# Kernel optimization log

Measured on AMD Instinct MI355X. Metric: run time of the kernel, lower is better.

The kernel has to match this reference:

```python
import jax, jax.numpy as jnp
import numpy as np
import math

H = 8
D_MODEL = 32
D_HEAD = 4
FACTOR = 5
EPS = 1e-5

DATANUM = 1024
B = 512            # outer batch; becomes attention sequence length
C = 32
L = DATANUM // 8   # 128; becomes attention batch
U = min(FACTOR * int(math.ceil(math.log(B))), B)  # 35 (U_part == u since L_Q == L_K == B)


def setup_inputs() -> dict:
    key = jax.random.key(0)
    ks = jax.random.split(key, 16)
    s = 0.05
    return {
        'x': jax.random.normal(ks[0], (B, C, L), jnp.float32),
        'Wq': jax.random.normal(ks[1], (D_MODEL, D_MODEL), jnp.float32) * s,
        'bq': jnp.zeros((D_MODEL,), jnp.float32),
        'Wk': jax.random.normal(ks[2], (D_MODEL, D_MODEL), jnp.float32) * s,
        'bk': jnp.zeros((D_MODEL,), jnp.float32),
        'Wv': jax.random.normal(ks[3], (D_MODEL, D_MODEL), jnp.float32) * s,
        'bv': jnp.zeros((D_MODEL,), jnp.float32),
        'Wo': jax.random.normal(ks[4], (D_MODEL, D_MODEL), jnp.float32) * s,
        'bo': jnp.zeros((D_MODEL,), jnp.float32),
        'bn1_gamma': jnp.ones((C,), jnp.float32),
        'bn1_beta': jnp.zeros((C,), jnp.float32),
        'bn1_mean': jnp.zeros((C,), jnp.float32),
        'bn1_var': jnp.ones((C,), jnp.float32),
        'W1': jax.random.normal(ks[5], (DATANUM * 8, DATANUM * 4), jnp.float32) * 0.01,
        'b1': jnp.zeros((DATANUM * 8,), jnp.float32),
        'W2': jax.random.normal(ks[6], (DATANUM * 4, DATANUM * 8), jnp.float32) * 0.01,
        'b2': jnp.zeros((DATANUM * 4,), jnp.float32),
        'bn2_gamma': jnp.ones((C,), jnp.float32),
        'bn2_beta': jnp.zeros((C,), jnp.float32),
        'bn2_mean': jnp.zeros((C,), jnp.float32),
        'bn2_var': jnp.ones((C,), jnp.float32),
        'index_sample': jax.random.randint(ks[7], (B, U), 0, B, jnp.int64),
    }


def _bn(x, gamma, beta, mean, var):
    # eval-mode BatchNorm1d over channel dim of (batch, C, length)
    inv = jax.lax.rsqrt(var + EPS)
    return (x - mean[None, :, None]) * (inv * gamma)[None, :, None] + beta[None, :, None]


def _prob_attention(Q, K, V, index_sample):
    # Q,K,V: (Ba, H, Lq, D) self-attention, Lq == Lk. Informer ProbAttention, mask_flag=True.
    Ba, Hh, Lq, D = Q.shape
    u = index_sample.shape[1]
    # sparsity measurement on sampled keys
    K_sample = K[:, :, index_sample, :]                       # (Ba,H,Lq,U,D)
    QK_sample = jnp.einsum('bhld,bhlud->bhlu', Q, K_sample)
    M = QK_sample.max(axis=-1) - QK_sample.sum(axis=-1) / Lq  # (Ba,H,Lq)
    _, M_top = jax.lax.top_k(M, u)                            # (Ba,H,u) selected queries
    Q_reduce = jnp.take_along_axis(Q, M_top[..., None], axis=2)  # (Ba,H,u,D)
    scores = jnp.einsum('bhud,bhkd->bhuk', Q_reduce, K) / jnp.sqrt(jnp.float32(D))
    # ProbMask: causal w.r.t. the selected query's original position
    causal = jnp.arange(Lq)[None, None, None, :] > M_top[..., None]
    scores = jnp.where(causal, -jnp.inf, scores)
    attn = jax.nn.softmax(scores, axis=-1)
    upd = jnp.einsum('bhuk,bhkd->bhud', attn, V)              # (Ba,H,u,D)
    context = jnp.cumsum(V, axis=2)                           # initial context (mask_flag=True)
    b_idx = jnp.arange(Ba)[:, None, None]
    h_idx = jnp.arange(Hh)[None, :, None]
    context = context.at[b_idx, h_idx, M_top].set(upd)
    return context


def reference(x, Wq, bq, Wk, bk, Wv, bv, Wo, bo,
              bn1_gamma, bn1_beta, bn1_mean, bn1_var,
              W1, b1, W2, b2,
              bn2_gamma, bn2_beta, bn2_mean, bn2_var,
              index_sample):
    Bsz, Cc, Ll = x.shape
    res1 = x
    xa = jnp.transpose(x, (2, 0, 1))                          # (L, B, 32): attn batch=L, seq=B

    def heads(t):
        return jnp.transpose(t.reshape(Ll, Bsz, H, D_HEAD), (0, 2, 1, 3))

    Q = heads(xa @ Wq.T + bq)
    K = heads(xa @ Wk.T + bk)
    V = heads(xa @ Wv.T + bv)
    ctx = _prob_attention(Q, K, V, index_sample)              # (L,H,B,D)
    out = jnp.transpose(ctx, (0, 2, 1, 3)).reshape(Ll, Bsz, D_MODEL)
    out = out @ Wo.T + bo
    xh = jax.nn.relu(out)                                     # dropout = identity (eval)
    xh = jnp.transpose(xh, (1, 2, 0))                         # (B,32,L)
    xh = _bn(xh + res1, bn1_gamma, bn1_beta, bn1_mean, bn1_var)
    res2 = xh
    f = xh.reshape(Bsz, Cc * Ll)
    f = jax.nn.relu(f @ W1.T + b1)
    f = jax.nn.relu(f @ W2.T + b2)
    f = f.reshape(Bsz, Cc, Ll)
    return _bn(f + res2, bn2_gamma, bn2_beta, bn2_mean, bn2_var)
```

## Files before the change

kernel.cpp:

```cpp
#include <hip/hip_runtime.h>
#include <stdint.h>

#define EPSF 1e-5f
#define NEG_INF (-1e30f)

typedef float f32x4 __attribute__((ext_vector_type(4)));
typedef __bf16 bf16x8 __attribute__((ext_vector_type(8)));
typedef unsigned short u16x8 __attribute__((ext_vector_type(8)));

typedef __attribute__((address_space(3))) unsigned char* as3_ptr;
typedef const __attribute__((address_space(1))) unsigned char* as1_ptr;

__device__ __forceinline__ void async16(const void* g, void* l) {
  __builtin_amdgcn_global_load_lds((as1_ptr)g, (as3_ptr)l, 16, 0, 0);
}

__device__ __forceinline__ unsigned short f2bf(float f) {
  union { float f; unsigned int u; } v; v.f = f;
  unsigned int r = v.u + 0x7FFFu + ((v.u >> 16) & 1u);
  return (unsigned short)(r >> 16);
}
__device__ __forceinline__ unsigned short f2bf_fast(float f) {
  union { float f; unsigned int u; } v; v.f = f;
  return (unsigned short)((v.u + 0x8000u) >> 16);
}

__global__ __launch_bounds__(256) void transpose_k(const float* __restrict__ src,
                                                   float* __restrict__ dst, int R, int C) {
  __shared__ float tl[32][33];
  int tx = threadIdx.x & 31, ty = threadIdx.x >> 5;
  int c0 = blockIdx.x * 32, r0 = blockIdx.y * 32;
#pragma unroll
  for (int i = 0; i < 4; i++)
    tl[ty + i * 8][tx] = src[(size_t)(r0 + ty + i * 8) * C + c0 + tx];
  __syncthreads();
#pragma unroll
  for (int i = 0; i < 4; i++)
    dst[(size_t)(c0 + ty + i * 8) * R + r0 + tx] = tl[tx][ty + i * 8];
}

__global__ __launch_bounds__(256) void qkv_k(const float* __restrict__ xT,
    const float* __restrict__ Wq, const float* __restrict__ bq,
    const float* __restrict__ Wk, const float* __restrict__ bk,
    const float* __restrict__ Wv, const float* __restrict__ bv,
    float* __restrict__ Q, float* __restrict__ Kq, float* __restrict__ Vq) {
  __shared__ float xs[64 * 33];
  __shared__ float wq[32 * 33], wk[32 * 33], wvs[32 * 33];
  __shared__ float bqs[32], bks[32], bvs[32];
  int tid = threadIdx.x;
  int a = blockIdx.x;
  int tbase = blockIdx.y * 256;
#pragma unroll
  for (int i = 0; i < 4; i++) {
    int e = i * 256 + tid; int r = e >> 5, c = e & 31;
    wq[r * 33 + c] = Wq[e]; wk[r * 33 + c] = Wk[e]; wvs[r * 33 + c] = Wv[e];
  }
  if (tid < 32) { bqs[tid] = bq[tid]; bks[tid] = bk[tid]; bvs[tid] = bv[tid]; }
  int tl = tid & 63, rg = tid >> 6;
  for (int ch = 0; ch < 4; ch++) {
    __syncthreads();
#pragma unroll
    for (int i = 0; i < 8; i++) {
      int e = i * 256 + tid; int r = e >> 5, c = e & 31;
      xs[r * 33 + c] = xT[(size_t)a * 16384 + (size_t)(tbase + ch * 64) * 32 + e];
    }
    __syncthreads();
    float qa[8], ka[8], va[8];
#pragma unroll
    for (int r8 = 0; r8 < 8; r8++) {
      int r = rg * 8 + r8; qa[r8] = bqs[r]; ka[r8] = bks[r]; va[r8] = bvs[r];
    }
    for (int c = 0; c < 32; c++) {
      float xv = xs[tl * 33 + c];
#pragma unroll
      for (int r8 = 0; r8 < 8; r8++) {
        int r = rg * 8 + r8;
        qa[r8] += xv * wq[r * 33 + c];
        ka[r8] += xv * wk[r * 33 + c];
        va[r8] += xv * wvs[r * 33 + c];
      }
    }
    int t = tbase + ch * 64 + tl;
#pragma unroll
    for (int r8 = 0; r8 < 8; r8++) {
      int r = rg * 8 + r8;
      size_t o = (size_t)a * 16384 + (size_t)r * 512 + t;
      Q[o] = qa[r8]; Kq[o] = ka[r8]; Vq[o] = va[r8];
    }
  }
}

__global__ __launch_bounds__(512) void topk_k(const float* __restrict__ Q,
    const float* __restrict__ Kq, const int* __restrict__ idxs,
    int* __restrict__ Mtop, int U) {
  __shared__ float Ks[2048];
  __shared__ float Ml[512];
  __shared__ float rv[8];
  __shared__ int ri[8];
  int bh = blockIdx.x;
  int tid = threadIdx.x, lane = tid & 63, wv = tid >> 6;
  size_t base = (size_t)bh * 2048;
#pragma unroll
  for (int i = 0; i < 4; i++) Ks[i * 512 + tid] = Kq[base + i * 512 + tid];
  float q0 = Q[base + tid], q1 = Q[base + 512 + tid];
  float q2 = Q[base + 1024 + tid], q3 = Q[base + 1536 + tid];
  __syncthreads();
  float mx = NEG_INF, sm = 0.f;
  for (int u = 0; u < U; u++) {
    int it = idxs[tid * U + u];
    it = min(max(it, 0), 511);
    float s = q0 * Ks[it] + q1 * Ks[512 + it] + q2 * Ks[1024 + it] + q3 * Ks[1536 + it];
    mx = fmaxf(mx, s); sm += s;
  }
  Ml[tid] = mx - sm * (1.f / 512.f);
  __syncthreads();
  for (int s_i = 0; s_i < U; s_i++) {
    float v = Ml[tid]; int ii = tid;
#pragma unroll
    for (int off = 32; off; off >>= 1) {
      float ov = __shfl_xor(v, off); int oi = __shfl_xor(ii, off);
      if (ov > v || (ov == v && oi < ii)) { v = ov; ii = oi; }
    }
    if (lane == 0) { rv[wv] = v; ri[wv] = ii; }
    __syncthreads();
    if (tid == 0) {
      float bv = rv[0]; int bi = ri[0];
      for (int w = 1; w < 8; w++)
        if (rv[w] > bv || (rv[w] == bv && ri[w] < bi)) { bv = rv[w]; bi = ri[w]; }
      Mtop[bh * U + s_i] = bi;
      Ml[bi] = NEG_INF;
    }
    __syncthreads();
  }
}

__global__ __launch_bounds__(256) void attn_k(const float* __restrict__ Q,
    const float* __restrict__ Kq, const float* __restrict__ Vq,
    const int* __restrict__ Mtop, float* __restrict__ Ctx, int U) {
  __shared__ float Ks[2048];
  __shared__ float Vs[2048];
  __shared__ int mt[64];
  __shared__ float Qr[64][4];
  __shared__ float upd[64][4];
  int bh = blockIdx.x;
  int tid = threadIdx.x, lane = tid & 63, wv = tid >> 6;
  size_t base = (size_t)bh * 2048;
#pragma unroll
  for (int i = 0; i < 8; i++) {
    Ks[i * 256 + tid] = Kq[base + i * 256 + tid];
    Vs[i * 256 + tid] = Vq[base + i * 256 + tid];
  }
  if (tid < U) mt[tid] = Mtop[bh * U + tid];
  __syncthreads();
  if (tid < 4 * U) { int u = tid >> 2, d = tid & 3; Qr[u][d] = Q[base + d * 512 + mt[u]]; }
  __syncthreads();
  for (int u = wv; u < U; u += 4) {
    int mrow = mt[u];
    float q0 = Qr[u][0], q1 = Qr[u][1], q2 = Qr[u][2], q3 = Qr[u][3];
    float sv[8]; float lmax = NEG_INF;
#pragma unroll
    for (int jj = 0; jj < 8; jj++) {
      int k = jj * 64 + lane;
      float s = NEG_INF;
      if (k <= mrow)
        s = 0.5f * (q0 * Ks[k] + q1 * Ks[512 + k] + q2 * Ks[1024 + k] + q3 * Ks[1536 + k]);
      sv[jj] = s; lmax = fmaxf(lmax, s);
    }
#pragma unroll
    for (int off = 32; off; off >>= 1) lmax = fmaxf(lmax, __shfl_xor(lmax, off));
    float ls = 0.f, p0 = 0.f, p1 = 0.f, p2 = 0.f, p3 = 0.f;
#pragma unroll
    for (int jj = 0; jj < 8; jj++) {
      int k = jj * 64 + lane;
      if (k <= mrow) {
        float p = __expf(sv[jj] - lmax);
        ls += p; p0 += p * Vs[k]; p1 += p * Vs[512 + k];
        p2 += p * Vs[1024 + k]; p3 += p * Vs[1536 + k];
      }
    }
#pragma unroll
    for (int off = 32; off; off >>= 1) {
      ls += __shfl_xor(ls, off); p0 += __shfl_xor(p0, off); p1 += __shfl_xor(p1, off);
      p2 += __shfl_xor(p2, off); p3 += __shfl_xor(p3, off);
    }
    if (lane == 0) {
      float inv = 1.f / ls;
      upd[u][0] = p0 * inv; upd[u][1] = p1 * inv; upd[u][2] = p2 * inv; upd[u][3] = p3 * inv;
    }
  }
  __syncthreads();
  {
    float v[8];
    int b0 = wv * 512 + lane * 8;
#pragma unroll
    for (int q = 0; q < 8; q++) v[q] = Vs[b0 + q];
#pragma unroll
    for (int q = 1; q < 8; q++) v[q] += v[q - 1];
    float x = v[7];
    for (int off = 1; off < 64; off <<= 1) {
      float y = __shfl_up(x, off);
      if (lane >= off) x += y;
    }
    float excl = x - v[7];
#pragma unroll
    for (int q = 0; q < 8; q++) Vs[b0 + q] = v[q] + excl;
  }
  __syncthreads();
  if (tid < 4 * U) { int u = tid >> 2, d = tid & 3; Vs[d * 512 + mt[u]] = upd[u][d]; }
  __syncthreads();
#pragma unroll
  for (int i = 0; i < 8; i++) Ctx[base + i * 256 + tid] = Vs[i * 256 + tid];
}

__global__ __launch_bounds__(256) void oproj_k(const float* __restrict__ Ctx,
    const float* __restrict__ Wo, const float* __restrict__ bo, float* __restrict__ Y) {
  __shared__ float cs[32 * 256];
  __shared__ float wo[32 * 33];
  __shared__ float bos[32];
  int tid = threadIdx.x;
  int a = blockIdx.x, t0 = blockIdx.y * 256;
#pragma unroll
  for (int i = 0; i < 4; i++) {
    int e = i * 256 + tid; int r = e >> 5, c = e & 31;
    wo[r * 33 + c] = Wo[e];
  }
  if (tid < 32) bos[tid] = bo[tid];
#pragma unroll
  for (int i = 0; i < 32; i++) {
    int e = i * 256 + tid; int row = e >> 8, col = e & 255;
    cs[e] = Ctx[(size_t)a * 16384 + (size_t)row * 512 + t0 + col];
  }
  __syncthreads();
  int rl = tid & 31, tw = tid >> 5;
  for (int ti = 0; ti < 32; ti++) {
    int t = ti * 8 + tw;
    float acc = bos[rl];
#pragma unroll
    for (int rp = 0; rp < 32; rp++) acc += cs[rp * 256 + t] * wo[rl * 33 + rp];
    Y[(size_t)a * 16384 + (size_t)(t0 + t) * 32 + rl] = acc;
  }
}

__global__ __launch_bounds__(256) void bn1t_k(const float* __restrict__ Y,
    const float* __restrict__ x, const float* __restrict__ g1, const float* __restrict__ be1,
    const float* __restrict__ me1, const float* __restrict__ va1,
    float* __restrict__ Xh, unsigned short* __restrict__ Fb) {
  __shared__ float tl[32][33];
  int tx = threadIdx.x & 31, ty = threadIdx.x >> 5;
  int c0 = blockIdx.x * 32;
  int r0 = blockIdx.y * 32;
#pragma unroll
  for (int i = 0; i < 4; i++)
    tl[ty + i * 8][tx] = Y[(size_t)(r0 + ty + i * 8) * 16384 + c0 + tx];
  __syncthreads();
#pragma unroll
  for (int i = 0; i < 4; i++) {
    int m = c0 + ty + i * 8;
    int a = r0 + tx;
    float v = tl[tx][ty + i * 8];
    int ch = m & 31;
    size_t oi = (size_t)m * 128 + a;
    float val = fmaxf(v, 0.f) + x[oi];
    float s = g1[ch] * rsqrtf(va1[ch] + EPSF);
    float res = (val - me1[ch]) * s + be1[ch];
    Xh[oi] = res;
    Fb[oi] = f2bf(res);
  }
}

__global__ __launch_bounds__(256) void wcvt_k(const float* __restrict__ W,
    unsigned short* __restrict__ Wb, int n4) {
  int stride = gridDim.x * 256;
  for (int idx = blockIdx.x * 256 + threadIdx.x; idx < n4; idx += stride) {
    float4 w = ((const float4*)W)[idx];
    ushort4 o;
    o.x = f2bf(w.x); o.y = f2bf(w.y); o.z = f2bf(w.z); o.w = f2bf(w.w);
    ((ushort4*)Wb)[idx] = o;
  }
}

__global__ __launch_bounds__(256, 3) void gemm_bf(
    const unsigned short* __restrict__ A, const unsigned short* __restrict__ B,
    int K, int N, int MT, int NPX, int SPLITK, float* __restrict__ P, int M) {
  __shared__ unsigned char lds[16384];
  int tid = threadIdx.x;
  int lane = tid & 63, wv = tid >> 6;
  int wm = wv >> 1, wn = wv & 1;
  int lin = blockIdx.x;
  int xcd = lin & 7, slot = lin >> 3;
  int tilesPerSp = MT * NPX;
  int sp = slot / tilesPerSp;
  int rem = slot % tilesPerSp;
  int mt = rem % MT;
  int nt = xcd * NPX + rem / MT;
  int mtile0 = mt * 128, ntile0 = nt * 128;
  int m0 = mtile0 + wm * 64, n0 = ntile0 + wn * 64;
  int frow = lane & 15, q = lane >> 4;

  int nk = K / (32 * SPLITK);
  int kbase = sp * (K / SPLITK);

  f32x4 acc[4][4];
#pragma unroll
  for (int i = 0; i < 4; i++)
#pragma unroll
    for (int j = 0; j < 4; j++) { f32x4 z = {0.f, 0.f, 0.f, 0.f}; acc[i][j] = z; }

  for (int k = 0; k < nk; k++) {
    int ks = kbase + k * 32;
#pragma unroll
    for (int i = 0; i < 2; i++) {
      int e = i * 256 + tid;
      int row = e >> 2;
      int g = (e & 3) ^ ((row >> 1) & 3);
      async16(A + (size_t)(mtile0 + row) * K + ks + g * 8, lds + i * 4096 + wv * 1024);
    }
#pragma unroll
    for (int i = 0; i < 2; i++) {
      int e = i * 256 + tid;
      int row = e >> 2;
      int g = (e & 3) ^ ((row >> 1) & 3);
      async16(B + (size_t)(ntile0 + row) * K + ks + g * 8,
              lds + 8192 + i * 4096 + wv * 1024);
    }
    __syncthreads();
    bf16x8 af[4], bfr[4];
#pragma unroll
    for (int i = 0; i < 4; i++) {
      int row = wm * 64 + i * 16 + frow;
      af[i] = *(const bf16x8*)(lds + row * 64 + ((q ^ ((row >> 1) & 3)) << 4));
    }
#pragma unroll
    for (int j = 0; j < 4; j++) {
      int row = wn * 64 + j * 16 + frow;
      bfr[j] = *(const bf16x8*)(lds + 8192 + row * 64 + ((q ^ ((row >> 1) & 3)) << 4));
    }
#pragma unroll
    for (int i = 0; i < 4; i++)
#pragma unroll
      for (int j = 0; j < 4; j++)
        acc[i][j] = __builtin_amdgcn_mfma_f32_16x16x32_bf16(af[i], bfr[j], acc[i][j], 0, 0, 0);
    __syncthreads();
  }

  float* pb = P + (size_t)sp * M * N;
#pragma unroll
  for (int i = 0; i < 4; i++)
#pragma unroll
    for (int j = 0; j < 4; j++) {
      int n = n0 + j * 16 + frow;
      int mb = m0 + i * 16 + (q << 2);
#pragma unroll
      for (int r = 0; r < 4; r++)
        pb[(size_t)(mb + r) * N + n] = acc[i][j][r];
    }
}

template <int MI, int NJ, int EPI>
__global__ __launch_bounds__(256) void gemm_ps(
    const unsigned short* __restrict__ A, const float* __restrict__ Bw,
    const float* __restrict__ bias, int K, int N, int MT, int NPX, int SPLITK,
    float* __restrict__ Pout, int M,
    unsigned short* __restrict__ Hout, const float* __restrict__ res2,
    const float* __restrict__ g2, const float* __restrict__ be2,
    const float* __restrict__ me2, const float* __restrict__ va2,
    float* __restrict__ Out) {
  constexpr int BM = MI * 32;
  constexpr int BN = NJ * 32;
  constexpr int ABYTES = BM * 32 * 2;
  constexpr int BBYTES = BN * 32 * 4;
  constexpr int SA = ABYTES / 4096;
  constexpr int SB = BBYTES / 4096;
  __shared__ unsigned char lds[ABYTES + BBYTES];
  int tid = threadIdx.x;
  int lane = tid & 63, wv = tid >> 6;
  int wm = wv >> 1, wn = wv & 1;
  int lin = blockIdx.x;
  int xcd = lin & 7, slot = lin >> 3;
  int tilesPerSp = MT * NPX;
  int sp = slot / tilesPerSp;
  int rem = slot % tilesPerSp;
  int mt = rem % MT;
  int nt = xcd * NPX + rem / MT;
  int m0 = mt * BM + wm * (BM / 2);
  int n0 = nt * BN + wn * (BN / 2);
  int frow = lane & 15, q = lane >> 4;
  int nk = K / (32 * SPLITK);
  int kbase = sp * (K / SPLITK);
  f32x4 acc[MI][NJ];
#pragma unroll
  for (int i = 0; i < MI; i++)
#pragma unroll
    for (int j = 0; j < NJ; j++) { f32x4 z = {0.f, 0.f, 0.f, 0.f}; acc[i][j] = z; }
  int mtile0 = mt * BM, ntile0 = nt * BN;
  for (int k = 0; k < nk; k++) {
    int ks = kbase + k * 32;
#pragma unroll
    for (int i = 0; i < SA; i++) {
      int e = i * 256 + tid;
      int row = e >> 2;
      int g = (e & 3) ^ ((row >> 1) & 3);
      async16(A + (size_t)(mtile0 + row) * K + ks + g * 8, lds + i * 4096 + wv * 1024);
    }
#pragma unroll
    for (int i = 0; i < SB; i++) {
      int e = i * 256 + tid;
      int row = e >> 3;
      int g = (e & 7) ^ (row & 7);
      async16(Bw + (size_t)(ntile0 + row) * K + ks + g * 4,
              lds + ABYTES + i * 4096 + wv * 1024);
    }
    __syncthreads();
    bf16x8 af[MI];
    bf16x8 bfr[NJ];
#pragma unroll
    for (int i = 0; i < MI; i++) {
      int row = wm * (BM / 2) + i * 16 + frow;
      af[i] = *(const bf16x8*)(lds + row * 64 + ((q ^ ((row >> 1) & 3)) << 4));
    }
#pragma unroll
    for (int j = 0; j < NJ; j++) {
      int row = wn * (BN / 2) + j * 16 + frow;
      const unsigned char* rb = lds + ABYTES + row * 128;
      int sw = row & 7;
      float4 w0 = *(const float4*)(rb + (((2 * q + 0) ^ sw) << 4));
      float4 w1 = *(const float4*)(rb + (((2 * q + 1) ^ sw) << 4));
      union { u16x8 u; bf16x8 b; } cv;
      cv.u[0] = f2bf_fast(w0.x); cv.u[1] = f2bf_fast(w0.y);
      cv.u[2] = f2bf_fast(w0.z); cv.u[3] = f2bf_fast(w0.w);
      cv.u[4] = f2bf_fast(w1.x); cv.u[5] = f2bf_fast(w1.y);
      cv.u[6] = f2bf_fast(w1.z); cv.u[7] = f2bf_fast(w1.w);
      bfr[j] = cv.b;
    }
#pragma unroll
    for (int i = 0; i < MI; i++)
#pragma unroll
      for (int j = 0; j < NJ; j++)
        acc[i][j] = __builtin_amdgcn_mfma_f32_16x16x32_bf16(af[i], bfr[j], acc[i][j], 0, 0, 0);
    __syncthreads();
  }
#pragma unroll
  for (int i = 0; i < MI; i++)
#pragma unroll
    for (int j = 0; j < NJ; j++) {
      int n = n0 + j * 16 + frow;
      int mb = m0 + i * 16 + (q << 2);
      if constexpr (EPI == 2) {
        float* pb = Pout + (size_t)sp * M * N;
#pragma unroll
        for (int r = 0; r < 4; r++)
          pb[(size_t)(mb + r) * N + n] = acc[i][j][r];
      } else if constexpr (EPI == 0) {
        float bb = bias[n];
#pragma unroll
        for (int r = 0; r < 4; r++) {
          float v = fmaxf(acc[i][j][r] + bb, 0.f);
          Hout[(size_t)(mb + r) * N + n] = f2bf(v);
        }
      } else {
        float bb = bias[n];
        int ch = n >> 7;
        float s = g2[ch] * rsqrtf(va2[ch] + EPSF);
        float mu = me2[ch], bt = be2[ch];
#pragma unroll
        for (int r = 0; r < 4; r++) {
          float v = fmaxf(acc[i][j][r] + bb, 0.f);
          size_t oi = (size_t)(mb + r) * N + n;
          v += res2[oi];
          Out[oi] = (v - mu) * s + bt;
        }
      }
    }
}

template <int EPI>
__global__ __launch_bounds__(256) void red_k(const float* __restrict__ P, int SP,
    const float* __restrict__ bias, const float* __restrict__ Xh,
    const float* __restrict__ g2, const float* __restrict__ be2,
    const float* __restrict__ me2, const float* __restrict__ va2,
    unsigned short* __restrict__ H, float* __restrict__ Out, int N, int MN) {
  int idx = blockIdx.x * 256 + threadIdx.x;
  const float4* p = (const float4*)P;
  int mn4 = MN >> 2;
  float4 s = p[idx];
  for (int sp = 1; sp < SP; sp++) {
    float4 t = p[idx + (size_t)sp * mn4];
    s.x += t.x; s.y += t.y; s.z += t.z; s.w += t.w;
  }
  int n = (idx << 2) & (N - 1);
  float4 bb = *(const float4*)(bias + n);
  if constexpr (EPI == 0) {
    ushort4 o;
    o.x = f2bf(fmaxf(s.x + bb.x, 0.f));
    o.y = f2bf(fmaxf(s.y + bb.y, 0.f));
    o.z = f2bf(fmaxf(s.z + bb.z, 0.f));
    o.w = f2bf(fmaxf(s.w + bb.w, 0.f));
    ((ushort4*)H)[idx] = o;
  } else {
    int ch = n >> 7;
    float sc = g2[ch] * rsqrtf(va2[ch] + EPSF);
    float mu = me2[ch], bt = be2[ch];
    float4 xh = ((const float4*)Xh)[idx];
    float4 o;
    o.x = (fmaxf(s.x + bb.x, 0.f) + xh.x - mu) * sc + bt;
    o.y = (fmaxf(s.y + bb.y, 0.f) + xh.y - mu) * sc + bt;
    o.z = (fmaxf(s.z + bb.z, 0.f) + xh.z - mu) * sc + bt;
    o.w = (fmaxf(s.w + bb.w, 0.f) + xh.w - mu) * sc + bt;
    ((float4*)Out)[idx] = o;
  }
}

extern "C" void kernel_launch(void* const* d_in, const int* in_sizes, int n_in,
                              void* d_out, int out_size, void* d_ws, size_t ws_size,
                              hipStream_t stream) {
  const float* x  = (const float*)d_in[0];
  const float* Wq = (const float*)d_in[1];  const float* bq = (const float*)d_in[2];
  const float* Wk = (const float*)d_in[3];  const float* bk = (const float*)d_in[4];
  const float* Wv = (const float*)d_in[5];  const float* bv = (const float*)d_in[6];
  const float* Wo = (const float*)d_in[7];  const float* bo = (const float*)d_in[8];
  const float* g1 = (const float*)d_in[9];  const float* be1 = (const float*)d_in[10];
  const float* me1 = (const float*)d_in[11]; const float* va1 = (const float*)d_in[12];
  const float* W1 = (const float*)d_in[13]; const float* b1 = (const float*)d_in[14];
  const float* W2 = (const float*)d_in[15]; const float* b2 = (const float*)d_in[16];
  const float* g2 = (const float*)d_in[17]; const float* be2 = (const float*)d_in[18];
  const float* me2 = (const float*)d_in[19]; const float* va2 = (const float*)d_in[20];
  const int* idxs = (const int*)d_in[21];
  int U = in_sizes[21] / 512;
  float* out = (float*)d_out;

  char* ws = (char*)d_ws;
  float* QC = (float*)(ws);
  float* Kb = (float*)(ws + (8u << 20));
  float* Vb = (float*)(ws + (16u << 20));
  float* YT = (float*)(ws + (24u << 20));
  float* Xh = (float*)(ws + (32u << 20));
  int* Mtop = (int*)(ws + (40u << 20));
  unsigned short* Fb = (unsigned short*)Vb;
  unsigned short* Hb = (unsigned short*)Kb;
  unsigned short* Wb = (unsigned short*)(ws + (48u << 20));
  float* PA = (float*)(ws + (112u << 20));
  float* P1 = (float*)(ws + (48u << 20));
  float* P2 = (float*)(ws + (80u << 20));
  bool tierA = ws_size >= (size_t)176 * (1u << 20);
  bool tierB = !tierA && ws_size >= (size_t)112 * (1u << 20);

  dim3 b256(256);
  transpose_k<<<dim3(4, 512), b256, 0, stream>>>(x, YT, 16384, 128);
  qkv_k<<<dim3(128, 2), b256, 0, stream>>>(YT, Wq, bq, Wk, bk, Wv, bv, QC, Kb, Vb);
  topk_k<<<dim3(1024), dim3(512), 0, stream>>>(QC, Kb, idxs, Mtop, U);
  attn_k<<<dim3(1024), b256, 0, stream>>>(QC, Kb, Vb, Mtop, QC, U);
  oproj_k<<<dim3(128, 2), b256, 0, stream>>>(QC, Wo, bo, YT);
  bn1t_k<<<dim3(512, 4), b256, 0, stream>>>(YT, x, g1, be1, me1, va1, Xh, Fb);

  if (tierA) {
    wcvt_k<<<dim3(2048), b256, 0, stream>>>(W1, Wb, (8192 * 4096) / 4);
    gemm_bf<<<dim3(1024), b256, 0, stream>>>(Fb, Wb, 4096, 8192, 4, 8, 4, PA, 512);
    red_k<0><<<dim3(4096), b256, 0, stream>>>(PA, 4, b1, nullptr, nullptr, nullptr,
                                              nullptr, nullptr, Hb, nullptr, 8192,
                                              512 * 8192);
    wcvt_k<<<dim3(2048), b256, 0, stream>>>(W2, Wb, (4096 * 8192) / 4);
    gemm_bf<<<dim3(1024), b256, 0, stream>>>(Hb, Wb, 8192, 4096, 4, 4, 8, PA, 512);
    red_k<1><<<dim3(2048), b256, 0, stream>>>(PA, 8, b2, Xh, g2, be2, me2, va2,
                                              nullptr, out, 4096, 512 * 4096);
  } else if (tierB) {
    gemm_ps<4, 2, 2><<<dim3(1024), b256, 0, stream>>>(
        Fb, W1, nullptr, 4096, 8192, 4, 16, 2, P1, 512,
        nullptr, nullptr, nullptr, nullptr, nullptr, nullptr, nullptr);
    red_k<0><<<dim3(4096), b256, 0, stream>>>(P1, 2, b1, nullptr, nullptr, nullptr,
                                              nullptr, nullptr, Hb, nullptr, 8192,
                                              512 * 8192);
    gemm_ps<4, 2, 2><<<dim3(1024), b256, 0, stream>>>(
        Hb, W2, nullptr, 8192, 4096, 4, 8, 4, P2, 512,
        nullptr, nullptr, nullptr, nullptr, nullptr, nullptr, nullptr);
    red_k<1><<<dim3(2048), b256, 0, stream>>>(P2, 4, b2, Xh, g2, be2, me2, va2,
                                              nullptr, out, 4096, 512 * 4096);
  } else {
    gemm_ps<4, 2, 0><<<dim3(512), b256, 0, stream>>>(
        Fb, W1, b1, 4096, 8192, 4, 16, 1, nullptr, 512,
        Hb, nullptr, nullptr, nullptr, nullptr, nullptr, nullptr);
    gemm_ps<4, 2, 1><<<dim3(256), b256, 0, stream>>>(
        Hb, W2, b2, 8192, 4096, 4, 8, 1, nullptr, 512,
        nullptr, Xh, g2, be2, me2, va2, out);
  }
}
```

Before: 590.0 us.

## Fuse top-k selection into attention kernel using rank-count selection

```diff
diff --git a/kernel.cpp b/kernel.cpp
--- a/kernel.cpp
+++ b/kernel.cpp
@@ -90,18 +90,23 @@
   }
 }
 
-__global__ __launch_bounds__(512) void topk_k(const float* __restrict__ Q,
-    const float* __restrict__ Kq, const int* __restrict__ idxs,
-    int* __restrict__ Mtop, int U) {
+__global__ __launch_bounds__(512) void topattn_k(const float* __restrict__ Q,
+    const float* __restrict__ Kq, const float* __restrict__ Vq,
+    const int* __restrict__ idxs, float* __restrict__ Ctx, int U) {
   __shared__ float Ks[2048];
+  __shared__ float Vs[2048];
   __shared__ float Ml[512];
-  __shared__ float rv[8];
-  __shared__ int ri[8];
+  __shared__ int mt[64];
+  __shared__ float Qr[64][4];
+  __shared__ float upd[64][4];
   int bh = blockIdx.x;
   int tid = threadIdx.x, lane = tid & 63, wv = tid >> 6;
   size_t base = (size_t)bh * 2048;
 #pragma unroll
-  for (int i = 0; i < 4; i++) Ks[i * 512 + tid] = Kq[base + i * 512 + tid];
+  for (int i = 0; i < 4; i++) {
+    Ks[i * 512 + tid] = Kq[base + i * 512 + tid];
+    Vs[i * 512 + tid] = Vq[base + i * 512 + tid];
+  }
   float q0 = Q[base + tid], q1 = Q[base + 512 + tid];
   float q2 = Q[base + 1024 + tid], q3 = Q[base + 1536 + tid];
   __syncthreads();
@@ -114,56 +119,29 @@
   }
   Ml[tid] = mx - sm * (1.f / 512.f);
   __syncthreads();
-  for (int s_i = 0; s_i < U; s_i++) {
-    float v = Ml[tid]; int ii = tid;
-#pragma unroll
-    for (int off = 32; off; off >>= 1) {
-      float ov = __shfl_xor(v, off); int oi = __shfl_xor(ii, off);
-      if (ov > v || (ov == v && oi < ii)) { v = ov; ii = oi; }
-    }
-    if (lane == 0) { rv[wv] = v; ri[wv] = ii; }
-    __syncthreads();
-    if (tid == 0) {
-      float bv = rv[0]; int bi = ri[0];
-      for (int w = 1; w < 8; w++)
-        if (rv[w] > bv || (rv[w] == bv && ri[w] < bi)) { bv = rv[w]; bi = ri[w]; }
-      Mtop[bh * U + s_i] = bi;
-      Ml[bi] = NEG_INF;
-    }
-    __syncthreads();
-  }
-}
-
-__global__ __launch_bounds__(256) void attn_k(const float* __restrict__ Q,
-    const float* __restrict__ Kq, const float* __restrict__ Vq,
-    const int* __restrict__ Mtop, float* __restrict__ Ctx, int U) {
-  __shared__ float Ks[2048];
-  __shared__ float Vs[2048];
-  __shared__ int mt[64];
-  __shared__ float Qr[64][4];
-  __shared__ float upd[64][4];
-  int bh = blockIdx.x;
-  int tid = threadIdx.x, lane = tid & 63, wv = tid >> 6;
-  size_t base = (size_t)bh * 2048;
-#pragma unroll
-  for (int i = 0; i < 8; i++) {
-    Ks[i * 256 + tid] = Kq[base + i * 256 + tid];
-    Vs[i * 256 + tid] = Vq[base + i * 256 + tid];
-  }
-  if (tid < U) mt[tid] = Mtop[bh * U + tid];
+  float mi = Ml[tid];
+  int rank = 0;
+  for (int j0 = 0; j0 < 512; j0 += 4) {
+    float4 m4 = *(const float4*)(Ml + j0);
+    rank += (m4.x > mi) || (m4.x == mi && (j0 + 0) < tid);
+    rank += (m4.y > mi) || (m4.y == mi && (j0 + 1) < tid);
+    rank += (m4.z > mi) || (m4.z == mi && (j0 + 2) < tid);
+    rank += (m4.w > mi) || (m4.w == mi && (j0 + 3) < tid);
+  }
+  if (rank < U) mt[rank] = tid;
   __syncthreads();
   if (tid < 4 * U) { int u = tid >> 2, d = tid & 3; Qr[u][d] = Q[base + d * 512 + mt[u]]; }
   __syncthreads();
-  for (int u = wv; u < U; u += 4) {
+  for (int u = wv; u < U; u += 8) {
     int mrow = mt[u];
-    float q0 = Qr[u][0], q1 = Qr[u][1], q2 = Qr[u][2], q3 = Qr[u][3];
+    float p0q = Qr[u][0], p1q = Qr[u][1], p2q = Qr[u][2], p3q = Qr[u][3];
     float sv[8]; float lmax = NEG_INF;
 #pragma unroll
     for (int jj = 0; jj < 8; jj++) {
       int k = jj * 64 + lane;
       float s = NEG_INF;
       if (k <= mrow)
-        s = 0.5f * (q0 * Ks[k] + q1 * Ks[512 + k] + q2 * Ks[1024 + k] + q3 * Ks[1536 + k]);
+        s = 0.5f * (p0q * Ks[k] + p1q * Ks[512 + k] + p2q * Ks[1024 + k] + p3q * Ks[1536 + k]);
       sv[jj] = s; lmax = fmaxf(lmax, s);
     }
 #pragma unroll
@@ -189,7 +167,7 @@
     }
   }
   __syncthreads();
-  {
+  if (wv < 4) {
     float v[8];
     int b0 = wv * 512 + lane * 8;
 #pragma unroll
@@ -209,7 +187,7 @@
   if (tid < 4 * U) { int u = tid >> 2, d = tid & 3; Vs[d * 512 + mt[u]] = upd[u][d]; }
   __syncthreads();
 #pragma unroll
-  for (int i = 0; i < 8; i++) Ctx[base + i * 256 + tid] = Vs[i * 256 + tid];
+  for (int i = 0; i < 4; i++) Ctx[base + i * 512 + tid] = Vs[i * 512 + tid];
 }
 
 __global__ __launch_bounds__(256) void oproj_k(const float* __restrict__ Ctx,
@@ -534,7 +512,6 @@
   float* Vb = (float*)(ws + (16u << 20));
   float* YT = (float*)(ws + (24u << 20));
   float* Xh = (float*)(ws + (32u << 20));
-  int* Mtop = (int*)(ws + (40u << 20));
   unsigned short* Fb = (unsigned short*)Vb;
   unsigned short* Hb = (unsigned short*)Kb;
   unsigned short* Wb = (unsigned short*)(ws + (48u << 20));
@@ -547,8 +524,7 @@
   dim3 b256(256);
   transpose_k<<<dim3(4, 512), b256, 0, stream>>>(x, YT, 16384, 128);
   qkv_k<<<dim3(128, 2), b256, 0, stream>>>(YT, Wq, bq, Wk, bk, Wv, bv, QC, Kb, Vb);
-  topk_k<<<dim3(1024), dim3(512), 0, stream>>>(QC, Kb, idxs, Mtop, U);
-  attn_k<<<dim3(1024), b256, 0, stream>>>(QC, Kb, Vb, Mtop, QC, U);
+  topattn_k<<<dim3(1024), dim3(512), 0, stream>>>(QC, Kb, Vb, idxs, QC, U);
   oproj_k<<<dim3(128, 2), b256, 0, stream>>>(QC, Wo, bo, YT);
   bn1t_k<<<dim3(512, 4), b256, 0, stream>>>(YT, x, g1, be1, me1, va1, Xh, Fb);
 
```

New measurement: 552.3 us. -6.4%, faster.
